# Optimization experiments

Measured on AMD Instinct MI355X. Metric: run time of the kernel, lower is better.

## Reference

```python
import jax, jax.numpy as jnp
import numpy as np

# Module hyperparameters (init_kwargs defaults)
FOV_RATIO = 0.3125
K_RATIO = 0.208
SALIENCY_BETA = 0.5

B, C, H, W = 32, 3, 512, 512


def setup_inputs() -> dict:
    key = jax.random.key(0)
    k1, k2, k3 = jax.random.split(key, 3)
    img = jax.random.uniform(k1, (B, C, H, W), jnp.float32) * 255.0  # uint8-range pixels
    gaze = jax.random.uniform(k2, (B, 2), jnp.float32) * (min(H, W) - 1)  # (x, y) inside image
    saliency = jax.random.uniform(k3, (B, 1, H, W), jnp.float32)
    return {"img": img, "gaze": gaze, "saliency": saliency}


def _bilinear_grid_sample(img, grid):
    # img: (B,C,H,W) float; grid: (B,H,W,2) normalized coords in [-1,1]
    # Matches F.grid_sample(mode='bilinear', padding_mode='zeros', align_corners=True)
    Bh, Ch, Hh, Wh = img.shape
    x = (grid[..., 0] + 1.0) * 0.5 * (Wh - 1)  # (B,H,W) pixel coords
    y = (grid[..., 1] + 1.0) * 0.5 * (Hh - 1)
    x0 = jnp.floor(x)
    y0 = jnp.floor(y)
    x1 = x0 + 1.0
    y1 = y0 + 1.0
    wx1 = x - x0
    wx0 = 1.0 - wx1
    wy1 = y - y0
    wy0 = 1.0 - wy1

    def gather_one(im, yi, xi):
        # im: (C,H,W); yi, xi: (H,W) float corner coords
        valid = (xi >= 0) & (xi <= Wh - 1) & (yi >= 0) & (yi <= Hh - 1)
        xc = jnp.clip(xi, 0, Wh - 1).astype(jnp.int32)
        yc = jnp.clip(yi, 0, Hh - 1).astype(jnp.int32)
        vals = im[:, yc, xc]  # (C,H,W)
        return vals * valid[None].astype(im.dtype)

    gather = jax.vmap(gather_one)
    v00 = gather(img, y0, x0)
    v01 = gather(img, y0, x1)
    v10 = gather(img, y1, x0)
    v11 = gather(img, y1, x1)
    w00 = (wy0 * wx0)[:, None]
    w01 = (wy0 * wx1)[:, None]
    w10 = (wy1 * wx0)[:, None]
    w11 = (wy1 * wx1)[:, None]
    return v00 * w00 + v01 * w01 + v10 * w10 + v11 * w11


def _forward_float(img, gaze, saliency):
    Bh, Ch, Hh, Wh = img.shape
    ys = jnp.arange(Hh, dtype=img.dtype)[None, :, None]  # (1,H,1)
    xs = jnp.arange(Wh, dtype=img.dtype)[None, None, :]  # (1,1,W)
    x_g = gaze[:, 0][:, None, None]  # (B,1,1)
    y_g = gaze[:, 1][:, None, None]
    dx = xs - x_g  # (B,H,W)
    dy = ys - y_g
    r = jnp.sqrt(dx * dx + dy * dy + 1e-6)

    S = saliency[:, 0]  # (B,H,W)
    S = S / (S.sum(axis=(1, 2), keepdims=True) + 1e-6)
    mean_r = jnp.sum(S * r, axis=(1, 2), keepdims=True)
    mean_r2 = jnp.sum(S * r * r, axis=(1, 2), keepdims=True)
    var_r = mean_r2 - mean_r * mean_r
    std_r = jnp.sqrt(jnp.clip(var_r, 0.0, None))
    r_max = r.max(axis=(1, 2), keepdims=True)
    spread_norm = std_r / r_max  # (B,1,1)

    base_size = min(Hh, Wh)
    fov = FOV_RATIO * base_size
    K = K_RATIO * base_size
    fov_eff = fov * (1.0 + SALIENCY_BETA * spread_norm)  # (B,1,1)

    # radial_quadratic_batch, branchless
    r_peri = (r + K) ** 2 / (2.0 * (fov_eff + K)) + (fov_eff - K) / 2.0
    r_tfm = jnp.where(r < fov_eff, r, r_peri)
    coef = r_max / (r_tfm.max(axis=(1, 2), keepdims=True) + 1e-6)
    r_new = coef * r_tfm

    dx_norm = dx / r
    dy_norm = dy / r
    X_new = x_g + dx_norm * r_new
    Y_new = y_g + dy_norm * r_new
    X_norm = X_new / (Wh - 1) * 2.0 - 1.0
    Y_norm = Y_new / (Hh - 1) * 2.0 - 1.0
    grid = jnp.stack((X_norm, Y_norm), axis=-1)  # (B,H,W,2)
    out = _bilinear_grid_sample(img, grid)
    return jnp.clip(out, 0.0, 255.0)


def reference(img, gaze, saliency):
    return _forward_float(img, gaze, saliency).astype(jnp.uint8)
```

## Files before the change

kernel.cpp:

```cpp
#include <hip/hip_runtime.h>

#define Bn 32
#define Cn 3
#define Hn 512
#define Wn 512
#define HWn (Hn * Wn)

#define FOVc 160.0f
#define Kc   106.496f

__global__ __launch_bounds__(256) void reduce_k(const float4* __restrict__ sal,
                                                const float* __restrict__ gaze,
                                                float* __restrict__ ws) {
    const int b = blockIdx.y;
    const float xg = gaze[2 * b + 0];
    const float yg = gaze[2 * b + 1];
    const int tid = threadIdx.x;
    const int idx0 = blockIdx.x * 256 + tid;
    const float4* sb = sal + (size_t)b * (HWn / 4);

    float sumS = 0.0f, sumSr = 0.0f, sumSr2 = 0.0f, rmax = 0.0f;

    for (int i = idx0; i < HWn / 4; i += 32 * 256) {
        float4 s4 = sb[i];
        const int pix = i * 4;
        const float y = (float)(pix >> 9);
        const float xbase = (float)(pix & 511);
        const float dy = y - yg;
        const float dy2 = dy * dy + 1e-6f;
        const float sv[4] = {s4.x, s4.y, s4.z, s4.w};
#pragma unroll
        for (int j = 0; j < 4; ++j) {
            const float dx = xbase + (float)j - xg;
            const float r = sqrtf(dx * dx + dy2);
            const float s = sv[j];
            sumS   += s;
            sumSr  += s * r;
            sumSr2 += s * r * r;
            rmax = fmaxf(rmax, r);
        }
    }

#pragma unroll
    for (int off = 32; off > 0; off >>= 1) {
        sumS   += __shfl_down(sumS, off);
        sumSr  += __shfl_down(sumSr, off);
        sumSr2 += __shfl_down(sumSr2, off);
        rmax = fmaxf(rmax, __shfl_down(rmax, off));
    }

    __shared__ float red[4][4];
    const int wave = tid >> 6, lane = tid & 63;
    if (lane == 0) {
        red[wave][0] = sumS; red[wave][1] = sumSr; red[wave][2] = sumSr2; red[wave][3] = rmax;
    }
    __syncthreads();
    if (tid == 0) {
        float a = 0, c = 0, d = 0, m = 0;
        for (int w = 0; w < 4; ++w) {
            a += red[w][0]; c += red[w][1]; d += red[w][2]; m = fmaxf(m, red[w][3]);
        }
        atomicAdd(&ws[b * 4 + 0], a);
        atomicAdd(&ws[b * 4 + 1], c);
        atomicAdd(&ws[b * 4 + 2], d);
        atomicMax(reinterpret_cast<int*>(&ws[b * 4 + 3]), __float_as_int(m));
    }
}

__global__ __launch_bounds__(256) void sample_k(const float* __restrict__ img,
                                                const float* __restrict__ gaze,
                                                const float* __restrict__ ws,
                                                int* __restrict__ out) {
    const int b = blockIdx.y;
    const int pix0 = (blockIdx.x * 256 + threadIdx.x) * 4;

    const float xg = gaze[2 * b + 0];
    const float yg = gaze[2 * b + 1];

    const float sumS   = ws[b * 4 + 0];
    const float sumSr  = ws[b * 4 + 1];
    const float sumSr2 = ws[b * 4 + 2];
    const float rmax   = ws[b * 4 + 3];
    const float inv = 1.0f / (sumS + 1e-6f);
    const float mean_r  = sumSr * inv;
    const float mean_r2 = sumSr2 * inv;
    const float var_r = fmaxf(mean_r2 - mean_r * mean_r, 0.0f);
    const float spread = sqrtf(var_r) / rmax;
    const float fov_eff = FOVc * (1.0f + 0.5f * spread);
    float tmax;
    if (rmax < fov_eff) {
        tmax = rmax;
    } else {
        const float rk = rmax + Kc;
        tmax = rk * rk / (2.0f * (fov_eff + Kc)) + (fov_eff - Kc) * 0.5f;
    }
    const float coef = rmax / (tmax + 1e-6f);
    const float inv2fk = 0.5f / (fov_eff + Kc);
    const float addc   = (fov_eff - Kc) * 0.5f;

    const float y  = (float)(pix0 >> 9);
    const float xb = (float)(pix0 & 511);
    const float dy = y - yg;
    const float dy2 = dy * dy + 1e-6f;

    float w00[4], w01[4], w10[4], w11[4];
    int   o00[4], o01[4], o10[4], o11[4];

#pragma unroll
    for (int j = 0; j < 4; ++j) {
        const float dx = xb + (float)j - xg;
        const float d2 = dx * dx + dy2;
        const float inv_r = __builtin_amdgcn_rsqf(d2);
        const float r = d2 * inv_r;

        const float rk = r + Kc;
        const float r_peri = rk * rk * inv2fk + addc;
        const float r_tfm = (r < fov_eff) ? r : r_peri;
        const float scale = coef * r_tfm * inv_r;

        const float X = xg + dx * scale;
        const float Y = yg + dy * scale;

        const float x0f = floorf(X), y0f = floorf(Y);
        const float x1f = x0f + 1.0f, y1f = y0f + 1.0f;
        const float wx1 = X - x0f, wx0 = 1.0f - wx1;
        const float wy1 = Y - y0f, wy0 = 1.0f - wy1;

        const bool vx0 = (x0f >= 0.0f) & (x0f <= 511.0f);
        const bool vx1 = (x1f >= 0.0f) & (x1f <= 511.0f);
        const bool vy0 = (y0f >= 0.0f) & (y0f <= 511.0f);
        const bool vy1 = (y1f >= 0.0f) & (y1f <= 511.0f);

        const int xi0 = (int)fminf(fmaxf(x0f, 0.0f), 511.0f);
        const int xi1 = (int)fminf(fmaxf(x1f, 0.0f), 511.0f);
        const int yi0 = (int)fminf(fmaxf(y0f, 0.0f), 511.0f);
        const int yi1 = (int)fminf(fmaxf(y1f, 0.0f), 511.0f);

        w00[j] = wy0 * wx0 * ((vy0 & vx0) ? 1.0f : 0.0f);
        w01[j] = wy0 * wx1 * ((vy0 & vx1) ? 1.0f : 0.0f);
        w10[j] = wy1 * wx0 * ((vy1 & vx0) ? 1.0f : 0.0f);
        w11[j] = wy1 * wx1 * ((vy1 & vx1) ? 1.0f : 0.0f);

        o00[j] = yi0 * Wn + xi0;
        o01[j] = yi0 * Wn + xi1;
        o10[j] = yi1 * Wn + xi0;
        o11[j] = yi1 * Wn + xi1;
    }

    const float* ib = img + (size_t)b * Cn * HWn;
#pragma unroll
    for (int c = 0; c < Cn; ++c) {
        const float* p = ib + (size_t)c * HWn;
        int4 res;
        float v0 = p[o00[0]] * w00[0] + p[o01[0]] * w01[0] + p[o10[0]] * w10[0] + p[o11[0]] * w11[0];
        float v1 = p[o00[1]] * w00[1] + p[o01[1]] * w01[1] + p[o10[1]] * w10[1] + p[o11[1]] * w11[1];
        float v2 = p[o00[2]] * w00[2] + p[o01[2]] * w01[2] + p[o10[2]] * w10[2] + p[o11[2]] * w11[2];
        float v3 = p[o00[3]] * w00[3] + p[o01[3]] * w01[3] + p[o10[3]] * w10[3] + p[o11[3]] * w11[3];
        res.x = (int)fminf(fmaxf(v0, 0.0f), 255.0f);
        res.y = (int)fminf(fmaxf(v1, 0.0f), 255.0f);
        res.z = (int)fminf(fmaxf(v2, 0.0f), 255.0f);
        res.w = (int)fminf(fmaxf(v3, 0.0f), 255.0f);
        *reinterpret_cast<int4*>(&out[((size_t)b * Cn + c) * HWn + pix0]) = res;
    }
}

extern "C" void kernel_launch(void* const* d_in, const int* in_sizes, int n_in,
                              void* d_out, int out_size, void* d_ws, size_t ws_size,
                              hipStream_t stream) {
    const float* img  = (const float*)d_in[0];
    const float* gaze = (const float*)d_in[1];
    const float* sal  = (const float*)d_in[2];
    int* out  = (int*)d_out;
    float* ws = (float*)d_ws;

    hipMemsetAsync(d_ws, 0, 128 * sizeof(float), stream);

    reduce_k<<<dim3(32, Bn), 256, 0, stream>>>((const float4*)sal, gaze, ws);
    sample_k<<<dim3(HWn / 1024, Bn), 256, 0, stream>>>(img, gaze, ws, out);
}
```

Measured before the change: 276.8 us.

## Use 2D pixel tiles in sampler and replace atomics with per-block partials

Result: faster. 246.6 us (-10.9%).

```diff
diff --git a/kernel.cpp b/kernel.cpp
--- a/kernel.cpp
+++ b/kernel.cpp
@@ -5,13 +5,14 @@
 #define Hn 512
 #define Wn 512
 #define HWn (Hn * Wn)
+#define RBLK 16
 
 #define FOVc 160.0f
 #define Kc   106.496f
 
 __global__ __launch_bounds__(256) void reduce_k(const float4* __restrict__ sal,
                                                 const float* __restrict__ gaze,
-                                                float* __restrict__ ws) {
+                                                float4* __restrict__ ws) {
     const int b = blockIdx.y;
     const float xg = gaze[2 * b + 0];
     const float yg = gaze[2 * b + 1];
@@ -21,7 +22,7 @@
 
     float sumS = 0.0f, sumSr = 0.0f, sumSr2 = 0.0f, rmax = 0.0f;
 
-    for (int i = idx0; i < HWn / 4; i += 32 * 256) {
+    for (int i = idx0; i < HWn / 4; i += RBLK * 256) {
         float4 s4 = sb[i];
         const int pix = i * 4;
         const float y = (float)(pix >> 9);
@@ -60,27 +61,25 @@
         for (int w = 0; w < 4; ++w) {
             a += red[w][0]; c += red[w][1]; d += red[w][2]; m = fmaxf(m, red[w][3]);
         }
-        atomicAdd(&ws[b * 4 + 0], a);
-        atomicAdd(&ws[b * 4 + 1], c);
-        atomicAdd(&ws[b * 4 + 2], d);
-        atomicMax(reinterpret_cast<int*>(&ws[b * 4 + 3]), __float_as_int(m));
+        ws[b * RBLK + blockIdx.x] = make_float4(a, c, d, m);
     }
 }
 
 __global__ __launch_bounds__(256) void sample_k(const float* __restrict__ img,
                                                 const float* __restrict__ gaze,
-                                                const float* __restrict__ ws,
+                                                const float4* __restrict__ ws,
                                                 int* __restrict__ out) {
-    const int b = blockIdx.y;
-    const int pix0 = (blockIdx.x * 256 + threadIdx.x) * 4;
+    const int b = blockIdx.z;
 
+    float sumS = 0.0f, sumSr = 0.0f, sumSr2 = 0.0f, rmax = 0.0f;
+#pragma unroll
+    for (int k = 0; k < RBLK; ++k) {
+        const float4 p = ws[b * RBLK + k];
+        sumS += p.x; sumSr += p.y; sumSr2 += p.z; rmax = fmaxf(rmax, p.w);
+    }
     const float xg = gaze[2 * b + 0];
     const float yg = gaze[2 * b + 1];
 
-    const float sumS   = ws[b * 4 + 0];
-    const float sumSr  = ws[b * 4 + 1];
-    const float sumSr2 = ws[b * 4 + 2];
-    const float rmax   = ws[b * 4 + 3];
     const float inv = 1.0f / (sumS + 1e-6f);
     const float mean_r  = sumSr * inv;
     const float mean_r2 = sumSr2 * inv;
@@ -98,69 +97,58 @@
     const float inv2fk = 0.5f / (fov_eff + Kc);
     const float addc   = (fov_eff - Kc) * 0.5f;
 
-    const float y  = (float)(pix0 >> 9);
-    const float xb = (float)(pix0 & 511);
-    const float dy = y - yg;
-    const float dy2 = dy * dy + 1e-6f;
+    const int tx = threadIdx.x & 31;
+    const int ty = threadIdx.x >> 5;
+    const int xi = blockIdx.x * 32 + tx;
+    const int yi = blockIdx.y * 8 + ty;
+    const int pix = yi * Wn + xi;
 
-    float w00[4], w01[4], w10[4], w11[4];
-    int   o00[4], o01[4], o10[4], o11[4];
+    const float dx = (float)xi - xg;
+    const float dy = (float)yi - yg;
+    const float d2 = dx * dx + dy * dy + 1e-6f;
+    const float inv_r = __builtin_amdgcn_rsqf(d2);
+    const float r = d2 * inv_r;
 
-#pragma unroll
-    for (int j = 0; j < 4; ++j) {
-        const float dx = xb + (float)j - xg;
-        const float d2 = dx * dx + dy2;
-        const float inv_r = __builtin_amdgcn_rsqf(d2);
-        const float r = d2 * inv_r;
+    const float rk = r + Kc;
+    const float r_peri = rk * rk * inv2fk + addc;
+    const float r_tfm = (r < fov_eff) ? r : r_peri;
+    const float scale = coef * r_tfm * inv_r;
 
-        const float rk = r + Kc;
-        const float r_peri = rk * rk * inv2fk + addc;
-        const float r_tfm = (r < fov_eff) ? r : r_peri;
-        const float scale = coef * r_tfm * inv_r;
+    const float X = xg + dx * scale;
+    const float Y = yg + dy * scale;
 
-        const float X = xg + dx * scale;
-        const float Y = yg + dy * scale;
+    const float x0f = floorf(X), y0f = floorf(Y);
+    const float x1f = x0f + 1.0f, y1f = y0f + 1.0f;
+    const float wx1 = X - x0f, wx0 = 1.0f - wx1;
+    const float wy1 = Y - y0f, wy0 = 1.0f - wy1;
 
-        const float x0f = floorf(X), y0f = floorf(Y);
-        const float x1f = x0f + 1.0f, y1f = y0f + 1.0f;
-        const float wx1 = X - x0f, wx0 = 1.0f - wx1;
-        const float wy1 = Y - y0f, wy0 = 1.0f - wy1;
+    const bool vx0 = (x0f >= 0.0f) & (x0f <= 511.0f);
+    const bool vx1 = (x1f >= 0.0f) & (x1f <= 511.0f);
+    const bool vy0 = (y0f >= 0.0f) & (y0f <= 511.0f);
+    const bool vy1 = (y1f >= 0.0f) & (y1f <= 511.0f);
 
-        const bool vx0 = (x0f >= 0.0f) & (x0f <= 511.0f);
-        const bool vx1 = (x1f >= 0.0f) & (x1f <= 511.0f);
-        const bool vy0 = (y0f >= 0.0f) & (y0f <= 511.0f);
-        const bool vy1 = (y1f >= 0.0f) & (y1f <= 511.0f);
+    const int xc0 = (int)fminf(fmaxf(x0f, 0.0f), 511.0f);
+    const int xc1 = (int)fminf(fmaxf(x1f, 0.0f), 511.0f);
+    const int yc0 = (int)fminf(fmaxf(y0f, 0.0f), 511.0f);
+    const int yc1 = (int)fminf(fmaxf(y1f, 0.0f), 511.0f);
 
-        const int xi0 = (int)fminf(fmaxf(x0f, 0.0f), 511.0f);
-        const int xi1 = (int)fminf(fmaxf(x1f, 0.0f), 511.0f);
-        const int yi0 = (int)fminf(fmaxf(y0f, 0.0f), 511.0f);
-        const int yi1 = (int)fminf(fmaxf(y1f, 0.0f), 511.0f);
+    const float w00 = wy0 * wx0 * ((vy0 & vx0) ? 1.0f : 0.0f);
+    const float w01 = wy0 * wx1 * ((vy0 & vx1) ? 1.0f : 0.0f);
+    const float w10 = wy1 * wx0 * ((vy1 & vx0) ? 1.0f : 0.0f);
+    const float w11 = wy1 * wx1 * ((vy1 & vx1) ? 1.0f : 0.0f);
 
-        w00[j] = wy0 * wx0 * ((vy0 & vx0) ? 1.0f : 0.0f);
-        w01[j] = wy0 * wx1 * ((vy0 & vx1) ? 1.0f : 0.0f);
-        w10[j] = wy1 * wx0 * ((vy1 & vx0) ? 1.0f : 0.0f);
-        w11[j] = wy1 * wx1 * ((vy1 & vx1) ? 1.0f : 0.0f);
-
-        o00[j] = yi0 * Wn + xi0;
-        o01[j] = yi0 * Wn + xi1;
-        o10[j] = yi1 * Wn + xi0;
-        o11[j] = yi1 * Wn + xi1;
-    }
+    const int o00 = yc0 * Wn + xc0;
+    const int o01 = yc0 * Wn + xc1;
+    const int o10 = yc1 * Wn + xc0;
+    const int o11 = yc1 * Wn + xc1;
 
     const float* ib = img + (size_t)b * Cn * HWn;
 #pragma unroll
     for (int c = 0; c < Cn; ++c) {
         const float* p = ib + (size_t)c * HWn;
-        int4 res;
-        float v0 = p[o00[0]] * w00[0] + p[o01[0]] * w01[0] + p[o10[0]] * w10[0] + p[o11[0]] * w11[0];
-        float v1 = p[o00[1]] * w00[1] + p[o01[1]] * w01[1] + p[o10[1]] * w10[1] + p[o11[1]] * w11[1];
-        float v2 = p[o00[2]] * w00[2] + p[o01[2]] * w01[2] + p[o10[2]] * w10[2] + p[o11[2]] * w11[2];
-        float v3 = p[o00[3]] * w00[3] + p[o01[3]] * w01[3] + p[o10[3]] * w10[3] + p[o11[3]] * w11[3];
-        res.x = (int)fminf(fmaxf(v0, 0.0f), 255.0f);
-        res.y = (int)fminf(fmaxf(v1, 0.0f), 255.0f);
-        res.z = (int)fminf(fmaxf(v2, 0.0f), 255.0f);
-        res.w = (int)fminf(fmaxf(v3, 0.0f), 255.0f);
-        *reinterpret_cast<int4*>(&out[((size_t)b * Cn + c) * HWn + pix0]) = res;
+        float v = p[o00] * w00 + p[o01] * w01 + p[o10] * w10 + p[o11] * w11;
+        v = fminf(fmaxf(v, 0.0f), 255.0f);
+        __builtin_nontemporal_store((int)v, &out[((size_t)b * Cn + c) * HWn + pix]);
     }
 }
 
@@ -170,11 +158,9 @@
     const float* img  = (const float*)d_in[0];
     const float* gaze = (const float*)d_in[1];
     const float* sal  = (const float*)d_in[2];
-    int* out  = (int*)d_out;
-    float* ws = (float*)d_ws;
+    int* out   = (int*)d_out;
+    float4* ws = (float4*)d_ws;
 
-    hipMemsetAsync(d_ws, 0, 128 * sizeof(float), stream);
-
-    reduce_k<<<dim3(32, Bn), 256, 0, stream>>>((const float4*)sal, gaze, ws);
-    sample_k<<<dim3(HWn / 1024, Bn), 256, 0, stream>>>(img, gaze, ws, out);
+    reduce_k<<<dim3(RBLK, Bn), 256, 0, stream>>>((const float4*)sal, gaze, ws);
+    sample_k<<<dim3(Wn / 32, Hn / 8, Bn), 256, 0, stream>>>(img, gaze, ws, out);
 }
```
